# Performance work log

Measured on AMD Instinct MI355X. Metric: run time of the kernel, lower is better.

## Reference

```python
import jax, jax.numpy as jnp
import numpy as np

TIME_PENALTY = 0.01
PONDER_EPS = 0.01
TIME_LIMIT = 16
BATCH, INPUT_SIZE, HIDDEN_SIZE = 4096, 1024, 1024


def setup_inputs() -> dict:
    key = jax.random.key(0)
    ks = jax.random.split(key, 8)
    s_in = 1.0 / np.sqrt(INPUT_SIZE + 1)
    s_h = 1.0 / np.sqrt(HIDDEN_SIZE)
    return {
        "inputs": jax.random.normal(ks[0], (BATCH, INPUT_SIZE), jnp.float32),
        "hidden": jax.random.normal(ks[1], (BATCH, HIDDEN_SIZE), jnp.float32),
        # RNNCell params (input size = INPUT_SIZE + 1 for the first-step flag)
        "W_ih": jax.random.uniform(ks[2], (HIDDEN_SIZE, INPUT_SIZE + 1), jnp.float32, -s_in, s_in),
        "b_ih": jax.random.uniform(ks[3], (HIDDEN_SIZE,), jnp.float32, -s_in, s_in),
        "W_hh": jax.random.uniform(ks[4], (HIDDEN_SIZE, HIDDEN_SIZE), jnp.float32, -s_h, s_h),
        "b_hh": jax.random.uniform(ks[5], (HIDDEN_SIZE,), jnp.float32, -s_h, s_h),
        # halting unit: Linear(hidden_size, 1), bias initialized to -1.0
        "W_halt": jax.random.uniform(ks[6], (1, HIDDEN_SIZE), jnp.float32, -s_h, s_h),
        "b_halt": jnp.full((1,), -1.0, jnp.float32),
    }


def _act_forward(inputs, hidden, W_ih, b_ih, W_hh, b_hh, W_halt, b_halt):
    B = inputs.shape[0]
    H = W_hh.shape[0]
    dt = inputs.dtype
    budget = jnp.asarray(1.0 - PONDER_EPS, dt)
    # input projection: the last input column is the first-step flag, so
    # step_inputs @ W_ih^T == inputs @ W_ih[:, :-1]^T + flag * W_ih[:, -1]
    x_base = inputs @ W_ih[:, :-1].T + b_ih  # (B, H)
    flag_col = W_ih[:, -1]                    # (H,)
    flags = (jnp.arange(TIME_LIMIT - 1) == 0).astype(dt)

    def step(carry, flag):
        h, halt_accum, cont, tot_h, tot_rem, tot_steps = carry
        h = jnp.tanh(x_base + flag * flag_col + h @ W_hh.T + b_hh)  # (B, H)
        step_halt = jax.nn.sigmoid(h @ W_halt.T + b_halt)           # (B, 1)
        masked_halt = jnp.where(cont, step_halt, 0.0)
        # halt accumulator is detached in the original (torch.no_grad)
        halt_accum = halt_accum + jax.lax.stop_gradient(masked_halt)
        ending = cont & (halt_accum + step_halt > budget)
        cont = cont & (~ending)
        tot_steps = tot_steps + cont.astype(dt)
        masked_rem = jnp.where(ending, 1.0 - halt_accum, 0.0)
        combined = masked_halt + masked_rem
        tot_h = tot_h + combined * h
        tot_rem = tot_rem + masked_halt
        return (h, halt_accum, cont, tot_h, tot_rem, tot_steps), None

    init = (
        hidden,
        jnp.zeros((B, 1), dt),
        jnp.ones((B, 1), bool),
        jnp.zeros((B, H), dt),
        jnp.zeros((B, 1), dt),
        jnp.zeros((B, 1), dt),
    )
    (h, halt_accum, cont, tot_h, tot_rem, tot_steps), _ = jax.lax.scan(step, init, flags)
    # for-else branch: elements still continuing after the loop get the remainder
    # (zero-contribution if everything halted early, matching the early break)
    tot_h = tot_h + jnp.where(cont, 1.0 - halt_accum, 0.0) * h
    ponder_cost = -TIME_PENALTY * tot_rem.mean()
    return tot_h, ponder_cost, tot_steps + 1.0


def reference(inputs, hidden, W_ih, b_ih, W_hh, b_hh, W_halt, b_halt):
    return _act_forward(inputs, hidden, W_ih, b_ih, W_hh, b_hh, W_halt, b_halt)
```

## Files before the change

kernel.cpp:

```cpp
#include <hip/hip_runtime.h>
#include <math.h>

#define BATCH 4096
#define HID   1024
#define KDIM  1024
#define NSTEP 15
#define KV    3072

#define TMM 128
#define TNN 64
#define LDAH 72

typedef _Float16 half8 __attribute__((ext_vector_type(8)));
typedef float floatx4 __attribute__((ext_vector_type(4)));

__device__ __forceinline__ _Float16 f16hi(float x) { return (_Float16)x; }

__global__ __launch_bounds__(256) void setup_kernel(
    const float* __restrict__ W_ih, const float* __restrict__ W_hh,
    _Float16* __restrict__ B3ih, _Float16* __restrict__ B3hh,
    float* __restrict__ flagcol, int* __restrict__ list0, int* __restrict__ counts,
    float* __restrict__ halt_accum, float* __restrict__ tot_rem) {
    int idx = blockIdx.x * 256 + threadIdx.x;
    int n = idx >> 10, k = idx & 1023;
    {
        float w = W_hh[idx];
        _Float16 hi = f16hi(w);
        _Float16 lo = (_Float16)(w - (float)hi);
        size_t base = (size_t)n * KV;
        B3hh[base + k] = hi; B3hh[base + 1024 + k] = lo; B3hh[base + 2048 + k] = hi;
    }
    {
        float w = W_ih[(size_t)n * 1025 + k];
        _Float16 hi = f16hi(w);
        _Float16 lo = (_Float16)(w - (float)hi);
        size_t base = (size_t)n * KV;
        B3ih[base + k] = hi; B3ih[base + 1024 + k] = lo; B3ih[base + 2048 + k] = hi;
    }
    if (idx < BATCH) { list0[idx] = idx; halt_accum[idx] = 0.f; tot_rem[idx] = 0.f; }
    if (idx < KDIM) flagcol[idx] = W_ih[(size_t)idx * 1025 + 1024];
    if (idx < 16) counts[idx] = (idx == 0) ? BATCH : 0;
}

__global__ __launch_bounds__(256) void split_kernel(
    const float* __restrict__ inputs, const float* __restrict__ hidden,
    _Float16* __restrict__ Ihi, _Float16* __restrict__ Ilo,
    _Float16* __restrict__ Hhi, _Float16* __restrict__ Hlo) {
    size_t idx = (size_t)blockIdx.x * 256 + threadIdx.x;
    float x = inputs[idx];
    _Float16 h = f16hi(x);
    Ihi[idx] = h; Ilo[idx] = (_Float16)(x - (float)h);
    float y = hidden[idx];
    _Float16 g = f16hi(y);
    Hhi[idx] = g; Hlo[idx] = (_Float16)(y - (float)g);
}

__global__ __launch_bounds__(256) void mfma_step_kernel(
    const _Float16* __restrict__ Ahi, const _Float16* __restrict__ Alo,
    const _Float16* __restrict__ B3, const float* __restrict__ bias,
    const float* __restrict__ xbase, const float* __restrict__ flagcol, float flag,
    const int* __restrict__ list, const int* __restrict__ pcount,
    float* __restrict__ hout, _Float16* __restrict__ houthi, _Float16* __restrict__ houtlo,
    float* __restrict__ xout, int mode) {
    int count = pcount ? *pcount : BATCH;
    int row0 = blockIdx.x * TMM;
    if (row0 >= count) return;
    int col0 = blockIdx.y * TNN;

    __shared__ _Float16 Asm[TMM][LDAH];
    __shared__ _Float16 Bsm[TNN][LDAH];

    int t = threadIdx.x;
    int lane = t & 63, w = t >> 6;
    int wm = (w & 1) * 64, wn = (w >> 1) * 32;

    int arw[4], aq8[4]; size_t aoff[4];
#pragma unroll
    for (int l = 0; l < 4; l++) {
        int q = t + l * 256;
        int r = q >> 3, qk = q & 7;
        arw[l] = r; aq8[l] = qk * 8;
        int rr = row0 + r;
        int g = (rr < count) ? (list ? list[rr] : rr) : 0;
        aoff[l] = (size_t)g * KDIM + qk * 8;
    }
    int brw[2], bq8[2]; size_t boff[2];
#pragma unroll
    for (int l = 0; l < 2; l++) {
        int q = t + l * 256;
        int r = q >> 3, qk = q & 7;
        brw[l] = r; bq8[l] = qk * 8;
        boff[l] = (size_t)(col0 + r) * KV + qk * 8;
    }

    floatx4 acc[4][2];
#pragma unroll
    for (int i = 0; i < 4; i++)
#pragma unroll
        for (int j = 0; j < 2; j++) acc[i][j] = (floatx4)(0.f);

    int l15 = lane & 15, l4 = lane >> 4;
    for (int it = 0; it < KV / 64; it++) {
        int k0v = it << 6;
        const _Float16* Asrc = (k0v < 2048) ? Ahi : Alo;
        int kp = k0v & 1023;
        half8 av[4], bv[2];
#pragma unroll
        for (int l = 0; l < 4; l++) av[l] = *(const half8*)(Asrc + aoff[l] + kp);
#pragma unroll
        for (int l = 0; l < 2; l++) bv[l] = *(const half8*)(B3 + boff[l] + k0v);
        __syncthreads();
#pragma unroll
        for (int l = 0; l < 4; l++) *(half8*)(&Asm[arw[l]][aq8[l]]) = av[l];
#pragma unroll
        for (int l = 0; l < 2; l++) *(half8*)(&Bsm[brw[l]][bq8[l]]) = bv[l];
        __syncthreads();
#pragma unroll
        for (int ks = 0; ks < 2; ks++) {
            int ko = ks * 32 + l4 * 8;
            half8 af[4], bf[2];
#pragma unroll
            for (int fi = 0; fi < 4; fi++)
                af[fi] = *(const half8*)(&Asm[wm + fi * 16 + l15][ko]);
#pragma unroll
            for (int fj = 0; fj < 2; fj++)
                bf[fj] = *(const half8*)(&Bsm[wn + fj * 16 + l15][ko]);
#pragma unroll
            for (int fi = 0; fi < 4; fi++)
#pragma unroll
                for (int fj = 0; fj < 2; fj++)
                    acc[fi][fj] = __builtin_amdgcn_mfma_f32_16x16x32_f16(
                        af[fi], bf[fj], acc[fi][fj], 0, 0, 0);
        }
    }

#pragma unroll
    for (int fi = 0; fi < 4; fi++) {
#pragma unroll
        for (int rr = 0; rr < 4; rr++) {
            int lm = wm + fi * 16 + l4 * 4 + rr;
            int grd = row0 + lm;
            if (grd >= count) continue;
            int g = list ? list[grd] : grd;
#pragma unroll
            for (int fj = 0; fj < 2; fj++) {
                int c = col0 + wn + fj * 16 + l15;
                float v = acc[fi][fj][rr];
                if (mode == 0) {
                    xout[(size_t)g * KDIM + c] = v + bias[c];
                } else {
                    v += xbase[(size_t)g * KDIM + c] + flag * flagcol[c] + bias[c];
                    v = tanhf(v);
                    hout[(size_t)g * KDIM + c] = v;
                    _Float16 hi = f16hi(v);
                    houthi[(size_t)g * KDIM + c] = hi;
                    houtlo[(size_t)g * KDIM + c] = (_Float16)(v - (float)hi);
                }
            }
        }
    }
}

__global__ __launch_bounds__(256) void halt_kernel(
    const float* __restrict__ h, const float* __restrict__ W_halt,
    const float* __restrict__ b_halt,
    const int* __restrict__ list, const int* __restrict__ pcount,
    int* __restrict__ list_next, int* __restrict__ pcount_next,
    float* __restrict__ halt_accum, float* __restrict__ tot_rem,
    float* __restrict__ tot_h, float* __restrict__ steps_out,
    int stepnum, int first) {
    int count = *pcount;
    int wid = threadIdx.x >> 6, lane = threadIdx.x & 63;
    int r = blockIdx.x * 4 + wid;
    if (r >= count) return;
    int row = list[r];
    const float* hr = h + (size_t)row * HID;

    float dot = 0.f;
#pragma unroll
    for (int q = 0; q < 4; q++) {
        int c = q * 256 + lane * 4;
        float4 hv = *(const float4*)(hr + c);
        float4 wv = *(const float4*)(W_halt + c);
        dot += hv.x * wv.x + hv.y * wv.y + hv.z * wv.z + hv.w * wv.w;
    }
#pragma unroll
    for (int off = 32; off > 0; off >>= 1) dot += __shfl_down(dot, off);

    float combined = 0.f;
    if (lane == 0) {
        float p = 1.f / (1.f + expf(-(dot + b_halt[0])));
        float S = halt_accum[row] + p;
        halt_accum[row] = S;
        tot_rem[row] += p;
        bool ending = (S + p) > 0.99f;
        if (ending) {
            combined = p + (1.f - S);
            steps_out[row] = (float)stepnum;
        } else {
            combined = p;
            int idx = atomicAdd(pcount_next, 1);
            list_next[idx] = row;
        }
    }
    combined = __shfl(combined, 0);

    float* th = tot_h + (size_t)row * HID;
#pragma unroll
    for (int q = 0; q < 4; q++) {
        int c = q * 256 + lane * 4;
        float4 hv = *(const float4*)(hr + c);
        float4 ov;
        if (first) {
            ov.x = combined * hv.x; ov.y = combined * hv.y;
            ov.z = combined * hv.z; ov.w = combined * hv.w;
        } else {
            ov = *(const float4*)(th + c);
            ov.x += combined * hv.x; ov.y += combined * hv.y;
            ov.z += combined * hv.z; ov.w += combined * hv.w;
        }
        *(float4*)(th + c) = ov;
    }
}

__global__ __launch_bounds__(256) void epilogue_kernel(
    const float* __restrict__ h, const int* __restrict__ list,
    const int* __restrict__ pcount, const float* __restrict__ halt_accum,
    const float* __restrict__ tot_rem,
    float* __restrict__ tot_h, float* __restrict__ steps_out,
    float* __restrict__ ponder) {
    if (blockIdx.x == 1024) {
        __shared__ float red[4];
        int t = threadIdx.x;
        float v = 0.f;
#pragma unroll
        for (int i = 0; i < 16; i++) v += tot_rem[t + i * 256];
#pragma unroll
        for (int off = 32; off > 0; off >>= 1) v += __shfl_down(v, off);
        int lane = t & 63, wid = t >> 6;
        if (lane == 0) red[wid] = v;
        __syncthreads();
        if (t == 0) ponder[0] = (red[0] + red[1] + red[2] + red[3]) * (-0.01f / 4096.f);
        return;
    }
    int count = *pcount;
    int wid = threadIdx.x >> 6, lane = threadIdx.x & 63;
    int r = blockIdx.x * 4 + wid;
    if (r >= count) return;
    int row = list[r];
    float cmb = 1.f - halt_accum[row];
    if (lane == 0) steps_out[row] = 16.f;
    const float* hr = h + (size_t)row * HID;
    float* th = tot_h + (size_t)row * HID;
#pragma unroll
    for (int q = 0; q < 4; q++) {
        int c = q * 256 + lane * 4;
        float4 hv = *(const float4*)(hr + c);
        float4 ov = *(const float4*)(th + c);
        ov.x += cmb * hv.x; ov.y += cmb * hv.y;
        ov.z += cmb * hv.z; ov.w += cmb * hv.w;
        *(float4*)(th + c) = ov;
    }
}

extern "C" void kernel_launch(void* const* d_in, const int* in_sizes, int n_in,
                              void* d_out, int out_size, void* d_ws, size_t ws_size,
                              hipStream_t stream) {
    const float* inputs = (const float*)d_in[0];
    const float* hidden = (const float*)d_in[1];
    const float* W_ih   = (const float*)d_in[2];
    const float* b_ih   = (const float*)d_in[3];
    const float* W_hh   = (const float*)d_in[4];
    const float* b_hh   = (const float*)d_in[5];
    const float* W_halt = (const float*)d_in[6];
    const float* b_halt = (const float*)d_in[7];
    float* out = (float*)d_out;

    float* ws = (float*)d_ws;
    const size_t NM = (size_t)BATCH * HID;
    float* xbase = ws;
    float* h     = xbase + NM;
    _Float16* B3ih = (_Float16*)(h + NM);
    _Float16* B3hh = B3ih + (size_t)HID * KV;
    _Float16* Ahi0 = B3hh + (size_t)HID * KV;
    _Float16* Alo0 = Ahi0 + NM;
    _Float16* Ahi1 = Alo0 + NM;
    _Float16* Alo1 = Ahi1 + NM;
    float* flagcol = (float*)(Alo1 + NM);
    float* halt_accum = flagcol + KDIM;
    float* tot_rem = halt_accum + BATCH;
    int* list0 = (int*)(tot_rem + BATCH);
    int* list1 = list0 + BATCH;
    int* counts = list1 + BATCH;

    _Float16* Ahi[2] = {Ahi0, Ahi1};
    _Float16* Alo[2] = {Alo0, Alo1};
    int* lists[2] = {list0, list1};

    float* tot_h = out;
    float* ponder = out + NM;
    float* steps_out = ponder + 1;

    setup_kernel<<<4096, 256, 0, stream>>>(W_ih, W_hh, B3ih, B3hh, flagcol,
                                           list0, counts, halt_accum, tot_rem);
    split_kernel<<<16384, 256, 0, stream>>>(inputs, hidden, Ahi1, Alo1, Ahi0, Alo0);

    mfma_step_kernel<<<dim3(32, 16), 256, 0, stream>>>(
        Ahi1, Alo1, B3ih, b_ih, nullptr, nullptr, 0.f, nullptr, nullptr,
        nullptr, nullptr, nullptr, xbase, 0);

    for (int t = 0; t < NSTEP; t++) {
        mfma_step_kernel<<<dim3(32, 16), 256, 0, stream>>>(
            Ahi[t & 1], Alo[t & 1], B3hh, b_hh, xbase, flagcol,
            (t == 0) ? 1.f : 0.f, lists[t & 1], counts + t,
            h, Ahi[(t + 1) & 1], Alo[(t + 1) & 1], nullptr, 1);
        halt_kernel<<<1024, 256, 0, stream>>>(h, W_halt, b_halt,
                                              lists[t & 1], counts + t,
                                              lists[(t + 1) & 1], counts + t + 1,
                                              halt_accum, tot_rem, tot_h, steps_out,
                                              t + 1, (t == 0) ? 1 : 0);
    }
    epilogue_kernel<<<1025, 256, 0, stream>>>(h, lists[1], counts + 15,
                                              halt_accum, tot_rem, tot_h, steps_out, ponder);
}
```

Measured before the change: 782.4 us.

## Double-buffer LDS tiles in MFMA GEMM and merge setup with split kernel

The step GEMM now uses two shared-memory buffers per operand, so the global loads for the next K chunk are issued before the MFMAs on the current chunk, and there is one barrier per iteration instead of two. This is meant to hide global-load latency behind matrix math. Separately, the input/hidden fp16 split kernel is folded into the weight setup kernel, removing one launch. The cost is double the LDS footprint, which may reduce occupancy, and extra live registers for the prefetched data.

```diff
diff --git a/kernel.cpp b/kernel.cpp
--- a/kernel.cpp
+++ b/kernel.cpp
@@ -6,6 +6,7 @@
 #define KDIM  1024
 #define NSTEP 15
 #define KV    3072
+#define NCHUNK (KV / 64)
 
 #define TMM 128
 #define TNN 64
@@ -18,41 +19,36 @@
 
 __global__ __launch_bounds__(256) void setup_kernel(
     const float* __restrict__ W_ih, const float* __restrict__ W_hh,
+    const float* __restrict__ inputs, const float* __restrict__ hidden,
     _Float16* __restrict__ B3ih, _Float16* __restrict__ B3hh,
+    _Float16* __restrict__ Ihi, _Float16* __restrict__ Ilo,
+    _Float16* __restrict__ Hhi, _Float16* __restrict__ Hlo,
     float* __restrict__ flagcol, int* __restrict__ list0, int* __restrict__ counts,
     float* __restrict__ halt_accum, float* __restrict__ tot_rem) {
-    int idx = blockIdx.x * 256 + threadIdx.x;
-    int n = idx >> 10, k = idx & 1023;
+    size_t idx = (size_t)blockIdx.x * 256 + threadIdx.x;
     {
+        float x = inputs[idx];
+        _Float16 h = f16hi(x);
+        Ihi[idx] = h; Ilo[idx] = (_Float16)(x - (float)h);
+        float y = hidden[idx];
+        _Float16 g = f16hi(y);
+        Hhi[idx] = g; Hlo[idx] = (_Float16)(y - (float)g);
+    }
+    if (idx < (size_t)KDIM * KDIM) {
+        int n = (int)(idx >> 10), k = (int)(idx & 1023);
         float w = W_hh[idx];
         _Float16 hi = f16hi(w);
         _Float16 lo = (_Float16)(w - (float)hi);
         size_t base = (size_t)n * KV;
         B3hh[base + k] = hi; B3hh[base + 1024 + k] = lo; B3hh[base + 2048 + k] = hi;
-    }
-    {
-        float w = W_ih[(size_t)n * 1025 + k];
-        _Float16 hi = f16hi(w);
-        _Float16 lo = (_Float16)(w - (float)hi);
-        size_t base = (size_t)n * KV;
-        B3ih[base + k] = hi; B3ih[base + 1024 + k] = lo; B3ih[base + 2048 + k] = hi;
+        float w2 = W_ih[(size_t)n * 1025 + k];
+        _Float16 hi2 = f16hi(w2);
+        _Float16 lo2 = (_Float16)(w2 - (float)hi2);
+        B3ih[base + k] = hi2; B3ih[base + 1024 + k] = lo2; B3ih[base + 2048 + k] = hi2;
     }
     if (idx < BATCH) { list0[idx] = idx; halt_accum[idx] = 0.f; tot_rem[idx] = 0.f; }
-    if (idx < KDIM) flagcol[idx] = W_ih[(size_t)idx * 1025 + 1024];
+    if (idx < KDIM) flagcol[idx] = W_ih[idx * 1025 + 1024];
     if (idx < 16) counts[idx] = (idx == 0) ? BATCH : 0;
-}
-
-__global__ __launch_bounds__(256) void split_kernel(
-    const float* __restrict__ inputs, const float* __restrict__ hidden,
-    _Float16* __restrict__ Ihi, _Float16* __restrict__ Ilo,
-    _Float16* __restrict__ Hhi, _Float16* __restrict__ Hlo) {
-    size_t idx = (size_t)blockIdx.x * 256 + threadIdx.x;
-    float x = inputs[idx];
-    _Float16 h = f16hi(x);
-    Ihi[idx] = h; Ilo[idx] = (_Float16)(x - (float)h);
-    float y = hidden[idx];
-    _Float16 g = f16hi(y);
-    Hhi[idx] = g; Hlo[idx] = (_Float16)(y - (float)g);
 }
 
 __global__ __launch_bounds__(256) void mfma_step_kernel(
@@ -67,8 +63,8 @@
     if (row0 >= count) return;
     int col0 = blockIdx.y * TNN;
 
-    __shared__ _Float16 Asm[TMM][LDAH];
-    __shared__ _Float16 Bsm[TNN][LDAH];
+    __shared__ _Float16 Asm[2][TMM][LDAH];
+    __shared__ _Float16 Bsm[2][TNN][LDAH];
 
     int t = threadIdx.x;
     int lane = t & 63, w = t >> 6;
@@ -100,31 +96,39 @@
         for (int j = 0; j < 2; j++) acc[i][j] = (floatx4)(0.f);
 
     int l15 = lane & 15, l4 = lane >> 4;
-    for (int it = 0; it < KV / 64; it++) {
-        int k0v = it << 6;
-        const _Float16* Asrc = (k0v < 2048) ? Ahi : Alo;
-        int kp = k0v & 1023;
-        half8 av[4], bv[2];
-#pragma unroll
-        for (int l = 0; l < 4; l++) av[l] = *(const half8*)(Asrc + aoff[l] + kp);
-#pragma unroll
-        for (int l = 0; l < 2; l++) bv[l] = *(const half8*)(B3 + boff[l] + k0v);
-        __syncthreads();
-#pragma unroll
-        for (int l = 0; l < 4; l++) *(half8*)(&Asm[arw[l]][aq8[l]]) = av[l];
-#pragma unroll
-        for (int l = 0; l < 2; l++) *(half8*)(&Bsm[brw[l]][bq8[l]]) = bv[l];
-        __syncthreads();
+
+    half8 av[4], bv[2];
+#pragma unroll
+    for (int l = 0; l < 4; l++) av[l] = *(const half8*)(Ahi + aoff[l]);
+#pragma unroll
+    for (int l = 0; l < 2; l++) bv[l] = *(const half8*)(B3 + boff[l]);
+#pragma unroll
+    for (int l = 0; l < 4; l++) *(half8*)(&Asm[0][arw[l]][aq8[l]]) = av[l];
+#pragma unroll
+    for (int l = 0; l < 2; l++) *(half8*)(&Bsm[0][brw[l]][bq8[l]]) = bv[l];
+    __syncthreads();
+
+    int p = 0;
+    for (int it = 0; it < NCHUNK; it++) {
+        if (it + 1 < NCHUNK) {
+            int k0v = (it + 1) << 6;
+            const _Float16* Asrc = (k0v < 2048) ? Ahi : Alo;
+            int kp = k0v & 1023;
+#pragma unroll
+            for (int l = 0; l < 4; l++) av[l] = *(const half8*)(Asrc + aoff[l] + kp);
+#pragma unroll
+            for (int l = 0; l < 2; l++) bv[l] = *(const half8*)(B3 + boff[l] + k0v);
+        }
 #pragma unroll
         for (int ks = 0; ks < 2; ks++) {
             int ko = ks * 32 + l4 * 8;
             half8 af[4], bf[2];
 #pragma unroll
             for (int fi = 0; fi < 4; fi++)
-                af[fi] = *(const half8*)(&Asm[wm + fi * 16 + l15][ko]);
+                af[fi] = *(const half8*)(&Asm[p][wm + fi * 16 + l15][ko]);
 #pragma unroll
             for (int fj = 0; fj < 2; fj++)
-                bf[fj] = *(const half8*)(&Bsm[wn + fj * 16 + l15][ko]);
+                bf[fj] = *(const half8*)(&Bsm[p][wn + fj * 16 + l15][ko]);
 #pragma unroll
             for (int fi = 0; fi < 4; fi++)
 #pragma unroll
@@ -132,6 +136,15 @@
                     acc[fi][fj] = __builtin_amdgcn_mfma_f32_16x16x32_f16(
                         af[fi], bf[fj], acc[fi][fj], 0, 0, 0);
         }
+        if (it + 1 < NCHUNK) {
+            int q = p ^ 1;
+#pragma unroll
+            for (int l = 0; l < 4; l++) *(half8*)(&Asm[q][arw[l]][aq8[l]]) = av[l];
+#pragma unroll
+            for (int l = 0; l < 2; l++) *(half8*)(&Bsm[q][brw[l]][bq8[l]]) = bv[l];
+        }
+        __syncthreads();
+        p ^= 1;
     }
 
 #pragma unroll
@@ -301,9 +314,9 @@
     float* ponder = out + NM;
     float* steps_out = ponder + 1;
 
-    setup_kernel<<<4096, 256, 0, stream>>>(W_ih, W_hh, B3ih, B3hh, flagcol,
-                                           list0, counts, halt_accum, tot_rem);
-    split_kernel<<<16384, 256, 0, stream>>>(inputs, hidden, Ahi1, Alo1, Ahi0, Alo0);
+    setup_kernel<<<16384, 256, 0, stream>>>(W_ih, W_hh, inputs, hidden,
+                                            B3ih, B3hh, Ahi1, Alo1, Ahi0, Alo0,
+                                            flagcol, list0, counts, halt_accum, tot_rem);
 
     mfma_step_kernel<<<dim3(32, 16), 256, 0, stream>>>(
         Ahi1, Alo1, B3ih, b_ih, nullptr, nullptr, 0.f, nullptr, nullptr,
```

New measurement: 736.6 us. 5.9% less time.
